# Kernel tuning notes

Measured on AMD Instinct MI355X. Metric: run time of the kernel, lower is better.

The kernel has to match this reference:

```python
import jax, jax.numpy as jnp
import numpy as np
import math

S, B, D, H = 2048, 2, 1024, 16
DK = D // H

def setup_inputs() -> dict:
    key = jax.random.key(0)
    ks = jax.random.split(key, 32)
    f = lambda k, shape, s=1.0: jax.random.normal(k, shape, dtype=jnp.float32) * s
    inp = {
        'qx': f(ks[0], (S, B, D)),
        'kx': f(ks[1], (S, B, D)),
        'vx': f(ks[2], (S, B, D)),
        'qc': f(ks[3], (S, B, D)),
        'kc': f(ks[4], (S, B, D)),
    }
    w = 1.0 / math.sqrt(D)
    names = ['qx_lin', 'kx_lin', 'vx_lin', 'qc_lin', 'kc_lin', 'out_lin']
    for i, n in enumerate(names):
        inp['W_' + n] = f(ks[5 + 2 * i], (D, D), w)
        inp['b_' + n] = f(ks[6 + 2 * i], (D,), w)
    vnames = ['Vqx', 'Vqc', 'Vkx', 'Vkc']
    for i, n in enumerate(vnames):
        inp['W_' + n] = f(ks[17 + 2 * i], (D, 1), w)
        inp['b_' + n] = f(ks[18 + 2 * i], (1,), w)
    return inp

def _forward(qx, kx, vx, qc, kc,
             W_qx_lin, b_qx_lin, W_kx_lin, b_kx_lin, W_vx_lin, b_vx_lin,
             W_qc_lin, b_qc_lin, W_kc_lin, b_kc_lin, W_out_lin, b_out_lin,
             W_Vqx, b_Vqx, W_Vqc, b_Vqc, W_Vkx, b_Vkx, W_Vkc, b_Vkc):
    # [S,B,D] -> [B,S,D]
    qx = jnp.swapaxes(qx, 0, 1)
    kx = jnp.swapaxes(kx, 0, 1)
    vx = jnp.swapaxes(vx, 0, 1)
    qc = jnp.swapaxes(qc, 0, 1)
    kc = jnp.swapaxes(kc, 0, 1)
    bs = qx.shape[0]

    qx = qx @ W_qx_lin + b_qx_lin
    kx = kx @ W_kx_lin + b_kx_lin
    v = vx @ W_vx_lin + b_vx_lin
    qc = qc @ W_qc_lin + b_qc_lin
    kc = kc @ W_kc_lin + b_kc_lin

    lam_q = jax.nn.sigmoid((qx @ W_Vqx + b_Vqx) + (qc @ W_Vqc + b_Vqc))  # [B,S,1]
    lam_k = jax.nn.sigmoid((kx @ W_Vkx + b_Vkx) + (kc @ W_Vkc + b_Vkc))
    q = (1.0 - lam_q) * qx + lam_q * qc
    k = (1.0 - lam_k) * kx + lam_k * kc

    # [B,S,D] -> [B,H,S,dk]
    q = q.reshape(bs, -1, H, DK).transpose(0, 2, 1, 3)
    k = k.reshape(bs, -1, H, DK).transpose(0, 2, 1, 3)
    v = v.reshape(bs, -1, H, DK).transpose(0, 2, 1, 3)

    scores = jnp.einsum('bhqd,bhkd->bhqk', q, k) / math.sqrt(DK)
    attn = jax.nn.softmax(scores, axis=-1)  # dropout is identity in eval
    ctx = jnp.einsum('bhqk,bhkd->bhqd', attn, v)

    concat = ctx.transpose(0, 2, 1, 3).reshape(bs, -1, D)
    out = concat @ W_out_lin + b_out_lin
    return jnp.swapaxes(out, 0, 1)  # back to [S,B,D]

def reference(qx, kx, vx, qc, kc,
              W_qx_lin, b_qx_lin, W_kx_lin, b_kx_lin, W_vx_lin, b_vx_lin,
              W_qc_lin, b_qc_lin, W_kc_lin, b_kc_lin, W_out_lin, b_out_lin,
              W_Vqx, b_Vqx, W_Vqc, b_Vqc, W_Vkx, b_Vkx, W_Vkc, b_Vkc):
    return _forward(qx, kx, vx, qc, kc,
                    W_qx_lin, b_qx_lin, W_kx_lin, b_kx_lin, W_vx_lin, b_vx_lin,
                    W_qc_lin, b_qc_lin, W_kc_lin, b_kc_lin, W_out_lin, b_out_lin,
                    W_Vqx, b_Vqx, W_Vqc, b_Vqc, W_Vkx, b_Vkx, W_Vkc, b_Vkc)
```

## Files before the change

### kernel.cpp

```cpp
#include <hip/hip_runtime.h>
#include <math.h>

typedef unsigned short u16;
typedef __attribute__((ext_vector_type(8))) short short8;
typedef __attribute__((ext_vector_type(4))) float floatx4;
typedef __attribute__((ext_vector_type(4))) unsigned short ushort4v;
typedef __attribute__((ext_vector_type(2))) unsigned int uint2v;

__device__ __forceinline__ float bf2f(u16 x) {
    union { unsigned int u; float f; } v; v.u = ((unsigned int)x) << 16; return v.f;
}
__device__ __forceinline__ u16 f2bf(float f) {
    union { float f; unsigned int u; } v; v.f = f;
    unsigned int r = v.u + 0x7fffu + ((v.u >> 16) & 1u);
    return (u16)(r >> 16);
}
__device__ __forceinline__ unsigned int pk2bf(float a, float b) {
    return (unsigned int)f2bf(a) | ((unsigned int)f2bf(b) << 16);
}

__device__ __forceinline__ void gl_lds16(const void* g, void* l) {
    __builtin_amdgcn_global_load_lds(
        (const __attribute__((address_space(1))) unsigned int*)g,
        (__attribute__((address_space(3))) unsigned int*)l,
        16, 0, 0);
}

struct CastJobs { const float* src[5]; u16* dst[5]; };

__global__ __launch_bounds__(256) void castbf(CastJobs cj) {
    const int z = blockIdx.y;
    const size_t i = (size_t)blockIdx.x * 256 + threadIdx.x;
    const floatx4 v = *(const floatx4*)(cj.src[z] + i * 4);
    ushort4v o;
#pragma unroll
    for (int j = 0; j < 4; j++) o[j] = f2bf(v[j]);
    *(ushort4v*)(cj.dst[z] + i * 4) = o;
}

struct WTJobs { const float* src[6]; u16* dst[6]; };

__global__ __launch_bounds__(256) void wtrans(WTJobs wj) {
    __shared__ float tile[32][33];
    const int z = blockIdx.z;
    const float* W = wj.src[z];
    u16* Wt = wj.dst[z];
    const int n0 = blockIdx.x * 32, k0 = blockIdx.y * 32;
    const int tx = threadIdx.x & 31, ty = threadIdx.x >> 5;
#pragma unroll
    for (int i = 0; i < 4; i++)
        tile[ty + i * 8][tx] = W[(size_t)(k0 + ty + i * 8) * 1024 + n0 + tx];
    __syncthreads();
#pragma unroll
    for (int i = 0; i < 4; i++)
        Wt[(size_t)(n0 + ty + i * 8) * 1024 + k0 + tx] = f2bf(tile[tx][ty + i * 8]);
}

__global__ __launch_bounds__(256) void vtrans(const u16* __restrict__ V,
                                              u16* __restrict__ Vtg) {
    __shared__ u16 tile[32][34];
    const int bh = blockIdx.z, b = bh >> 4, h = bh & 15;
    const int base = b * 1024 + h * 64;
    const int s0 = blockIdx.x * 32, d0 = blockIdx.y * 32;
    const int tx = threadIdx.x & 31, ty = threadIdx.x >> 5;
#pragma unroll
    for (int i = 0; i < 4; i++)
        tile[ty + i * 8][tx] = V[(size_t)(s0 + ty + i * 8) * 2048 + base + d0 + tx];
    __syncthreads();
#pragma unroll
    for (int i = 0; i < 4; i++)
        Vtg[((size_t)bh * 64 + d0 + ty + i * 8) * 2048 + s0 + tx] = tile[tx][ty + i * 8];
}

struct GemmJob { const u16* A; const u16* Bt; const float* bias; u16* Cb; float* Cf; };
struct GemmJobs { GemmJob j[5]; };

__global__ __launch_bounds__(256, 2) void gemm_bt(GemmJobs jobs, int K, int N, int f32out) {
    __shared__ u16 As[128 * 32];
    __shared__ u16 Bs[128 * 32];
    const GemmJob jb = jobs.j[blockIdx.z];
    const int m0 = blockIdx.y * 128;
    const int n0 = blockIdx.x * 128;
    const int t = threadIdx.x;
    const int lane = t & 63;
    const int wid = t >> 6;
    const int wm = wid >> 1, wn = wid & 1;
    const int qd = lane >> 4, lm = lane & 15;

    const floatx4 zero4 = {0.f, 0.f, 0.f, 0.f};
    floatx4 acc[4][4];
#pragma unroll
    for (int i = 0; i < 4; i++)
#pragma unroll
        for (int j2 = 0; j2 < 4; j2++) acc[i][j2] = zero4;

    const u16* Ab = jb.A + (size_t)m0 * K;
    const u16* Bb = jb.Bt + (size_t)n0 * K;
    const int e0 = t * 8;
    const int r0 = e0 >> 5, c0 = e0 & 31;
    const int e1 = (256 + t) * 8;
    const int r1 = e1 >> 5, c1 = e1 & 31;

    for (int k0 = 0; k0 < K; k0 += 32) {
        __syncthreads();
        gl_lds16(Ab + (size_t)r0 * K + k0 + c0, &As[e0]);
        gl_lds16(Ab + (size_t)r1 * K + k0 + c1, &As[e1]);
        gl_lds16(Bb + (size_t)r0 * K + k0 + c0, &Bs[e0]);
        gl_lds16(Bb + (size_t)r1 * K + k0 + c1, &Bs[e1]);
        __syncthreads();

        short8 af[4], bfg[4];
#pragma unroll
        for (int i = 0; i < 4; i++) {
            af[i]  = *(const short8*)&As[(wm * 64 + i * 16 + lm) * 32 + qd * 8];
            bfg[i] = *(const short8*)&Bs[(wn * 64 + i * 16 + lm) * 32 + qd * 8];
        }
#pragma unroll
        for (int i = 0; i < 4; i++)
#pragma unroll
            for (int j2 = 0; j2 < 4; j2++)
                acc[i][j2] = __builtin_amdgcn_mfma_f32_16x16x32_bf16(af[i], bfg[j2], acc[i][j2], 0, 0, 0);
    }

#pragma unroll
    for (int i = 0; i < 4; i++) {
        const int mb = m0 + wm * 64 + i * 16 + qd * 4;
#pragma unroll
        for (int j2 = 0; j2 < 4; j2++) {
            const int col = n0 + wn * 64 + j2 * 16 + lm;
            const float bv = jb.bias[col];
            const floatx4 c = acc[i][j2];
            if (f32out) {
#pragma unroll
                for (int r = 0; r < 4; r++)
                    jb.Cf[(size_t)(mb + r) * N + col] = c[r] + bv;
            } else {
#pragma unroll
                for (int r = 0; r < 4; r++)
                    jb.Cb[(size_t)(mb + r) * N + col] = f2bf(c[r] + bv);
            }
        }
    }
}

__global__ __launch_bounds__(256) void gating(
    const u16* __restrict__ qxp, const u16* __restrict__ qcp,
    const u16* __restrict__ kxp, const u16* __restrict__ kcp,
    const float* __restrict__ wVqx, const float* __restrict__ wVqc,
    const float* __restrict__ wVkx, const float* __restrict__ wVkc,
    const float* __restrict__ bVqx, const float* __restrict__ bVqc,
    const float* __restrict__ bVkx, const float* __restrict__ bVkc,
    u16* __restrict__ qg, u16* __restrict__ kg) {
    const int row = blockIdx.x;
    const int z = blockIdx.y;
    const u16* xa = z ? kxp : qxp;
    const u16* xb = z ? kcp : qcp;
    const float* wa = z ? wVkx : wVqx;
    const float* wb = z ? wVkc : wVqc;
    const float bsum = z ? (bVkx[0] + bVkc[0]) : (bVqx[0] + bVqc[0]);
    u16* out = z ? kg : qg;

    const int t = threadIdx.x;
    const size_t off = (size_t)row * 1024 + t * 4;
    const ushort4v av = *(const ushort4v*)(xa + off);
    const ushort4v bv = *(const ushort4v*)(xb + off);
    const floatx4 wav = *(const floatx4*)(wa + t * 4);
    const floatx4 wbv = *(const floatx4*)(wb + t * 4);
    float afl[4], bfl[4];
    float part = 0.f;
#pragma unroll
    for (int j = 0; j < 4; j++) {
        afl[j] = bf2f(av[j]); bfl[j] = bf2f(bv[j]);
        part += afl[j] * wav[j] + bfl[j] * wbv[j];
    }
#pragma unroll
    for (int m = 1; m <= 32; m <<= 1) part += __shfl_xor(part, m);
    __shared__ float red[4];
    if ((t & 63) == 0) red[t >> 6] = part;
    __syncthreads();
    const float tot = red[0] + red[1] + red[2] + red[3] + bsum;
    const float lam = 1.f / (1.f + exp2f(-tot * 1.44269504f));
    ushort4v ov;
#pragma unroll
    for (int j = 0; j < 4; j++) ov[j] = f2bf(afl[j] + lam * (bfl[j] - afl[j]));
    *(ushort4v*)(out + off) = ov;
}

__global__ __launch_bounds__(256, 2) void attn2(
    const u16* __restrict__ Q, const u16* __restrict__ Kk,
    const u16* __restrict__ Vtg, u16* __restrict__ O) {
    __shared__ u16 Ks[64 * 72];
    __shared__ u16 Vs[64 * 72];
    __shared__ u16 Ps[4 * 32 * 72];

    const int bh = blockIdx.y, b = bh >> 4, h = bh & 15;
    const int base = b * 1024 + h * 64;
    const int t = threadIdx.x, lane = t & 63, w = t >> 6;
    const int qd = lane >> 4, lm = lane & 15;
    const int q0 = blockIdx.x * 128 + w * 32;

    short8 qf[2][2];
#pragma unroll
    for (int qh = 0; qh < 2; qh++) {
        const u16* qr = Q + (size_t)(q0 + qh * 16 + lm) * 2048 + base;
#pragma unroll
        for (int c = 0; c < 2; c++)
            qf[qh][c] = *(const short8*)(qr + c * 32 + qd * 8);
    }

    const floatx4 zero4 = {0.f, 0.f, 0.f, 0.f};
    floatx4 ctx[2][4];
#pragma unroll
    for (int qh = 0; qh < 2; qh++)
#pragma unroll
        for (int g = 0; g < 4; g++) ctx[qh][g] = zero4;
    float lpart[2] = {0.f, 0.f};

    u16* Pw = &Ps[w * 32 * 72];
    const float C = 0.18033688011112042f;

    const int sr = t >> 3, sc = (t & 7) * 8;
    const u16* ksrc = Kk + (size_t)sr * 2048 + base + sc;
    const u16* vsrc = Vtg + ((size_t)bh * 64 + sr) * 2048 + sc;
    u16* kdst0 = &Ks[sr * 72 + sc];
    u16* kdst1 = &Ks[(sr + 32) * 72 + sc];
    u16* vdst0 = &Vs[sr * 72 + sc];
    u16* vdst1 = &Vs[(sr + 32) * 72 + sc];

    for (int kt = 0; kt < 32; kt++) {
        __syncthreads();
        *(short8*)kdst0 = *(const short8*)ksrc;
        *(short8*)kdst1 = *(const short8*)(ksrc + (size_t)32 * 2048);
        *(short8*)vdst0 = *(const short8*)vsrc;
        *(short8*)vdst1 = *(const short8*)(vsrc + (size_t)32 * 2048);
        ksrc += (size_t)64 * 2048;
        vsrc += 64;
        __syncthreads();

#pragma unroll
        for (int g = 0; g < 4; g++) {
            const short8 kf0 = *(const short8*)&Ks[(g * 16 + lm) * 72 + qd * 8];
            const short8 kf1 = *(const short8*)&Ks[(g * 16 + lm) * 72 + 32 + qd * 8];
#pragma unroll
            for (int qh = 0; qh < 2; qh++) {
                floatx4 st = zero4;
                st = __builtin_amdgcn_mfma_f32_16x16x32_bf16(kf0, qf[qh][0], st, 0, 0, 0);
                st = __builtin_amdgcn_mfma_f32_16x16x32_bf16(kf1, qf[qh][1], st, 0, 0, 0);
                float p0 = exp2f(st[0] * C);
                float p1 = exp2f(st[1] * C);
                float p2 = exp2f(st[2] * C);
                float p3 = exp2f(st[3] * C);
                lpart[qh] += (p0 + p1) + (p2 + p3);
                uint2v pw;
                pw[0] = pk2bf(p0, p1);
                pw[1] = pk2bf(p2, p3);
                *(uint2v*)&Pw[(qh * 16 + lm) * 72 + g * 16 + qd * 4] = pw;
            }
        }

        short8 pa[2][2];
#pragma unroll
        for (int qh = 0; qh < 2; qh++)
#pragma unroll
            for (int c = 0; c < 2; c++)
                pa[qh][c] = *(const short8*)&Pw[(qh * 16 + lm) * 72 + c * 32 + qd * 8];
#pragma unroll
        for (int g = 0; g < 4; g++) {
            const short8 vb0 = *(const short8*)&Vs[(g * 16 + lm) * 72 + qd * 8];
            const short8 vb1 = *(const short8*)&Vs[(g * 16 + lm) * 72 + 32 + qd * 8];
#pragma unroll
            for (int qh = 0; qh < 2; qh++) {
                ctx[qh][g] = __builtin_amdgcn_mfma_f32_16x16x32_bf16(pa[qh][0], vb0, ctx[qh][g], 0, 0, 0);
                ctx[qh][g] = __builtin_amdgcn_mfma_f32_16x16x32_bf16(pa[qh][1], vb1, ctx[qh][g], 0, 0, 0);
            }
        }
    }

#pragma unroll
    for (int qh = 0; qh < 2; qh++) {
        float l = lpart[qh];
        l += __shfl_xor(l, 16);
        l += __shfl_xor(l, 32);
        float linv[4];
#pragma unroll
        for (int r = 0; r < 4; r++)
            linv[r] = 1.0f / __shfl(l, qd * 4 + r);
#pragma unroll
        for (int r = 0; r < 4; r++) {
            const int srow = q0 + qh * 16 + qd * 4 + r;
            u16* orow = O + (size_t)srow * 2048 + base;
#pragma unroll
            for (int g = 0; g < 4; g++)
                orow[g * 16 + lm] = f2bf(ctx[qh][g][r] * linv[r]);
        }
    }
}

extern "C" void kernel_launch(void* const* d_in, const int* in_sizes, int n_in,
                              void* d_out, int out_size, void* d_ws, size_t ws_size,
                              hipStream_t stream) {
    const float* qx = (const float*)d_in[0];
    const float* kx = (const float*)d_in[1];
    const float* vx = (const float*)d_in[2];
    const float* qc = (const float*)d_in[3];
    const float* kc = (const float*)d_in[4];
    const float* W_qx = (const float*)d_in[5];   const float* b_qx = (const float*)d_in[6];
    const float* W_kx = (const float*)d_in[7];   const float* b_kx = (const float*)d_in[8];
    const float* W_vx = (const float*)d_in[9];   const float* b_vx = (const float*)d_in[10];
    const float* W_qc = (const float*)d_in[11];  const float* b_qc = (const float*)d_in[12];
    const float* W_kc = (const float*)d_in[13];  const float* b_kc = (const float*)d_in[14];
    const float* W_out = (const float*)d_in[15]; const float* b_out = (const float*)d_in[16];
    const float* W_Vqx = (const float*)d_in[17]; const float* b_Vqx = (const float*)d_in[18];
    const float* W_Vqc = (const float*)d_in[19]; const float* b_Vqc = (const float*)d_in[20];
    const float* W_Vkx = (const float*)d_in[21]; const float* b_Vkx = (const float*)d_in[22];
    const float* W_Vkc = (const float*)d_in[23]; const float* b_Vkc = (const float*)d_in[24];

    char* ws = (char*)d_ws;
    const size_t NT = 4194304;
    const size_t XB_OFF = 0;
    const size_t WT_OFF = XB_OFF + 5 * NT * 2;
    const size_t P_OFF  = WT_OFF + 6 * 2097152;
    const size_t QG_OFF = P_OFF + 5 * NT * 2;
    const size_t KG_OFF = QG_OFF + NT * 2;
    const size_t CTX_OFF = KG_OFF + NT * 2;

    u16* Xb[5];
    for (int i = 0; i < 5; i++) Xb[i] = (u16*)(ws + XB_OFF + (size_t)i * NT * 2);
    u16* Wt[6];
    for (int i = 0; i < 6; i++) Wt[i] = (u16*)(ws + WT_OFF + (size_t)i * 2097152);
    u16* P[5];
    for (int i = 0; i < 5; i++) P[i] = (u16*)(ws + P_OFF + (size_t)i * NT * 2);
    u16* qg  = (u16*)(ws + QG_OFF);
    u16* kg  = (u16*)(ws + KG_OFF);
    u16* ctx = (u16*)(ws + CTX_OFF);
    u16* Vtg = (u16*)(ws + XB_OFF);

    CastJobs cj;
    const float* srcs[5] = {qx, kx, vx, qc, kc};
    for (int i = 0; i < 5; i++) { cj.src[i] = srcs[i]; cj.dst[i] = Xb[i]; }
    castbf<<<dim3(4096, 5), 256, 0, stream>>>(cj);

    WTJobs wj;
    const float* wsrc[6] = {W_qx, W_kx, W_vx, W_qc, W_kc, W_out};
    for (int i = 0; i < 6; i++) { wj.src[i] = wsrc[i]; wj.dst[i] = Wt[i]; }
    wtrans<<<dim3(32, 32, 6), 256, 0, stream>>>(wj);

    GemmJobs gj;
    const float* biases[5] = {b_qx, b_kx, b_vx, b_qc, b_kc};
    for (int i = 0; i < 5; i++) {
        gj.j[i].A = Xb[i]; gj.j[i].Bt = Wt[i]; gj.j[i].bias = biases[i];
        gj.j[i].Cb = P[i]; gj.j[i].Cf = nullptr;
    }
    gemm_bt<<<dim3(8, 32, 5), 256, 0, stream>>>(gj, 1024, 1024, 0);

    gating<<<dim3(4096, 2), 256, 0, stream>>>(P[0], P[3], P[1], P[4],
        W_Vqx, W_Vqc, W_Vkx, W_Vkc, b_Vqx, b_Vqc, b_Vkx, b_Vkc, qg, kg);

    vtrans<<<dim3(64, 2, 32), 256, 0, stream>>>(P[2], Vtg);

    attn2<<<dim3(16, 32), 256, 0, stream>>>(qg, kg, Vtg, ctx);

    GemmJobs gf;
    for (int i = 0; i < 5; i++) {
        gf.j[i].A = ctx; gf.j[i].Bt = Wt[5]; gf.j[i].bias = b_out;
        gf.j[i].Cb = nullptr; gf.j[i].Cf = (float*)d_out;
    }
    gemm_bt<<<dim3(8, 32, 1), 256, 0, stream>>>(gf, 1024, 1024, 1);
}
```

Baseline: 390.2 us.

## Fuse gating into dual projection GEMM and split attention over KV halves

Computes the gating lambdas algebraically: W·v is precomputed and dotted with the raw fp32 inputs in the cast kernel, so lambda is known before the projections. A new dual-GEMM kernel computes the x and c projections together and blends them in its epilogue. This removes the separate gating pass and the bf16 intermediates for q and k. Attention is split into two KV halves to double the grid, with a merge kernel that adds the fp32 partials, at the cost of extra fp32 traffic and two added launches. Lambda is now taken from fp32 inputs rather than bf16 projections, which slightly changes the numerics.

```diff
diff --git a/kernel.cpp b/kernel.cpp
--- a/kernel.cpp
+++ b/kernel.cpp
@@ -16,7 +16,12 @@
     return (u16)(r >> 16);
 }
 __device__ __forceinline__ unsigned int pk2bf(float a, float b) {
+#if __has_builtin(__builtin_amdgcn_cvt_pk_bf16_f32)
+    auto r = __builtin_amdgcn_cvt_pk_bf16_f32(a, b);
+    union { decltype(r) v; unsigned int u; } cv; cv.v = r; return cv.u;
+#else
     return (unsigned int)f2bf(a) | ((unsigned int)f2bf(b) << 16);
+#endif
 }
 
 __device__ __forceinline__ void gl_lds16(const void* g, void* l) {
@@ -26,16 +31,86 @@
         16, 0, 0);
 }
 
-struct CastJobs { const float* src[5]; u16* dst[5]; };
+struct WFuseJobs { const float* W[4]; const float* wv[4]; float* out[4]; };
+
+__global__ __launch_bounds__(256) void wfuse(WFuseJobs wf) {
+    const int z = blockIdx.y;
+    const float* W = wf.W[z];
+    const float* wv = wf.wv[z];
+    float* out = wf.out[z];
+    const int lane = threadIdx.x & 63, w = threadIdx.x >> 6;
+#pragma unroll
+    for (int i = 0; i < 4; i++) {
+        const int row = blockIdx.x * 16 + w * 4 + i;
+        const float* Wr = W + (size_t)row * 1024 + lane * 16;
+        const float* vr = wv + lane * 16;
+        float p = 0.f;
+#pragma unroll
+        for (int c = 0; c < 4; c++) {
+            const floatx4 a = *(const floatx4*)(Wr + c * 4);
+            const floatx4 b = *(const floatx4*)(vr + c * 4);
+            p += a[0] * b[0] + a[1] * b[1] + a[2] * b[2] + a[3] * b[3];
+        }
+#pragma unroll
+        for (int m = 1; m <= 32; m <<= 1) p += __shfl_xor(p, m);
+        if (lane == 0) out[row] = p;
+    }
+}
+
+struct CastJobs { const float* src[5]; u16* dst[5]; const float* w[5]; float* dot[5]; };
 
 __global__ __launch_bounds__(256) void castbf(CastJobs cj) {
     const int z = blockIdx.y;
-    const size_t i = (size_t)blockIdx.x * 256 + threadIdx.x;
+    const int row = blockIdx.x;
+    const int t = threadIdx.x;
+    const size_t i = (size_t)row * 256 + t;
     const floatx4 v = *(const floatx4*)(cj.src[z] + i * 4);
     ushort4v o;
 #pragma unroll
     for (int j = 0; j < 4; j++) o[j] = f2bf(v[j]);
     *(ushort4v*)(cj.dst[z] + i * 4) = o;
+
+    if (cj.w[z]) {
+        const floatx4 wv = *(const floatx4*)(cj.w[z] + t * 4);
+        float p = v[0] * wv[0] + v[1] * wv[1] + v[2] * wv[2] + v[3] * wv[3];
+#pragma unroll
+        for (int m = 1; m <= 32; m <<= 1) p += __shfl_xor(p, m);
+        __shared__ float red[4];
+        if ((t & 63) == 0) red[t >> 6] = p;
+        __syncthreads();
+        if (t == 0) cj.dot[z][row] = red[0] + red[1] + red[2] + red[3];
+    }
+}
+
+struct LamJobs {
+    const float* dA[2]; const float* dB[2];
+    const float* b1[2]; const float* b2[2];
+    const float* wv1[2]; const float* wv2[2];
+    const float* s1[2]; const float* s2[2];
+    float* lam[2];
+};
+
+__global__ __launch_bounds__(256) void lamk(LamJobs lj) {
+    const int z = blockIdx.y;
+    const int t = threadIdx.x;
+    float p = 0.f;
+    {
+        const floatx4 a1 = *(const floatx4*)(lj.b1[z] + t * 4);
+        const floatx4 w1 = *(const floatx4*)(lj.wv1[z] + t * 4);
+        const floatx4 a2 = *(const floatx4*)(lj.b2[z] + t * 4);
+        const floatx4 w2 = *(const floatx4*)(lj.wv2[z] + t * 4);
+#pragma unroll
+        for (int j = 0; j < 4; j++) p += a1[j] * w1[j] + a2[j] * w2[j];
+    }
+#pragma unroll
+    for (int m = 1; m <= 32; m <<= 1) p += __shfl_xor(p, m);
+    __shared__ float red[4];
+    if ((t & 63) == 0) red[t >> 6] = p;
+    __syncthreads();
+    const float c = red[0] + red[1] + red[2] + red[3] + lj.s1[z][0] + lj.s2[z][0];
+    const int row = blockIdx.x * 256 + t;
+    const float x = lj.dA[z][row] + lj.dB[z][row] + c;
+    lj.lam[z][row] = 1.f / (1.f + exp2f(-x * 1.44269504f));
 }
 
 struct WTJobs { const float* src[6]; u16* dst[6]; };
@@ -73,7 +148,7 @@
 }
 
 struct GemmJob { const u16* A; const u16* Bt; const float* bias; u16* Cb; float* Cf; };
-struct GemmJobs { GemmJob j[5]; };
+struct GemmJobs { GemmJob j[1]; };
 
 __global__ __launch_bounds__(256, 2) void gemm_bt(GemmJobs jobs, int K, int N, int f32out) {
     __shared__ u16 As[128 * 32];
@@ -143,57 +218,103 @@
     }
 }
 
-__global__ __launch_bounds__(256) void gating(
-    const u16* __restrict__ qxp, const u16* __restrict__ qcp,
-    const u16* __restrict__ kxp, const u16* __restrict__ kcp,
-    const float* __restrict__ wVqx, const float* __restrict__ wVqc,
-    const float* __restrict__ wVkx, const float* __restrict__ wVkc,
-    const float* __restrict__ bVqx, const float* __restrict__ bVqc,
-    const float* __restrict__ bVkx, const float* __restrict__ bVkc,
-    u16* __restrict__ qg, u16* __restrict__ kg) {
-    const int row = blockIdx.x;
-    const int z = blockIdx.y;
-    const u16* xa = z ? kxp : qxp;
-    const u16* xb = z ? kcp : qcp;
-    const float* wa = z ? wVkx : wVqx;
-    const float* wb = z ? wVkc : wVqc;
-    const float bsum = z ? (bVkx[0] + bVkc[0]) : (bVqx[0] + bVqc[0]);
-    u16* out = z ? kg : qg;
-
+struct FuseJob {
+    const u16* Aa; const u16* Ac; const u16* Ba; const u16* Bc;
+    const float* biasA; const float* biasC; const float* lam; u16* out;
+};
+struct FuseJobs { FuseJob j[2]; };
+
+__global__ __launch_bounds__(256, 2) void fusedproj(FuseJobs jobs) {
+    __shared__ u16 Asa[128 * 32];
+    __shared__ u16 Asc[128 * 32];
+    __shared__ u16 Bsa[128 * 32];
+    __shared__ u16 Bsc[128 * 32];
+    const FuseJob jb = jobs.j[blockIdx.z];
+    const int K = 1024;
+    const int m0 = blockIdx.y * 128;
+    const int n0 = blockIdx.x * 128;
     const int t = threadIdx.x;
-    const size_t off = (size_t)row * 1024 + t * 4;
-    const ushort4v av = *(const ushort4v*)(xa + off);
-    const ushort4v bv = *(const ushort4v*)(xb + off);
-    const floatx4 wav = *(const floatx4*)(wa + t * 4);
-    const floatx4 wbv = *(const floatx4*)(wb + t * 4);
-    float afl[4], bfl[4];
-    float part = 0.f;
-#pragma unroll
-    for (int j = 0; j < 4; j++) {
-        afl[j] = bf2f(av[j]); bfl[j] = bf2f(bv[j]);
-        part += afl[j] * wav[j] + bfl[j] * wbv[j];
-    }
-#pragma unroll
-    for (int m = 1; m <= 32; m <<= 1) part += __shfl_xor(part, m);
-    __shared__ float red[4];
-    if ((t & 63) == 0) red[t >> 6] = part;
-    __syncthreads();
-    const float tot = red[0] + red[1] + red[2] + red[3] + bsum;
-    const float lam = 1.f / (1.f + exp2f(-tot * 1.44269504f));
-    ushort4v ov;
-#pragma unroll
-    for (int j = 0; j < 4; j++) ov[j] = f2bf(afl[j] + lam * (bfl[j] - afl[j]));
-    *(ushort4v*)(out + off) = ov;
-}
-
-__global__ __launch_bounds__(256, 2) void attn2(
+    const int lane = t & 63;
+    const int wid = t >> 6;
+    const int wm = wid >> 1, wn = wid & 1;
+    const int qd = lane >> 4, lm = lane & 15;
+
+    const floatx4 zero4 = {0.f, 0.f, 0.f, 0.f};
+    floatx4 accA[4][4], accC[4][4];
+#pragma unroll
+    for (int i = 0; i < 4; i++)
+#pragma unroll
+        for (int j2 = 0; j2 < 4; j2++) { accA[i][j2] = zero4; accC[i][j2] = zero4; }
+
+    const u16* Aab = jb.Aa + (size_t)m0 * K;
+    const u16* Acb = jb.Ac + (size_t)m0 * K;
+    const u16* Bab = jb.Ba + (size_t)n0 * K;
+    const u16* Bcb = jb.Bc + (size_t)n0 * K;
+    const int e0 = t * 8;
+    const int r0 = e0 >> 5, c0 = e0 & 31;
+    const int e1 = (256 + t) * 8;
+    const int r1 = e1 >> 5, c1 = e1 & 31;
+
+    for (int k0 = 0; k0 < K; k0 += 32) {
+        __syncthreads();
+        gl_lds16(Aab + (size_t)r0 * K + k0 + c0, &Asa[e0]);
+        gl_lds16(Aab + (size_t)r1 * K + k0 + c1, &Asa[e1]);
+        gl_lds16(Acb + (size_t)r0 * K + k0 + c0, &Asc[e0]);
+        gl_lds16(Acb + (size_t)r1 * K + k0 + c1, &Asc[e1]);
+        gl_lds16(Bab + (size_t)r0 * K + k0 + c0, &Bsa[e0]);
+        gl_lds16(Bab + (size_t)r1 * K + k0 + c1, &Bsa[e1]);
+        gl_lds16(Bcb + (size_t)r0 * K + k0 + c0, &Bsc[e0]);
+        gl_lds16(Bcb + (size_t)r1 * K + k0 + c1, &Bsc[e1]);
+        __syncthreads();
+
+        short8 aa[4], ac[4], ba[4], bc[4];
+#pragma unroll
+        for (int i = 0; i < 4; i++) {
+            aa[i] = *(const short8*)&Asa[(wm * 64 + i * 16 + lm) * 32 + qd * 8];
+            ac[i] = *(const short8*)&Asc[(wm * 64 + i * 16 + lm) * 32 + qd * 8];
+            ba[i] = *(const short8*)&Bsa[(wn * 64 + i * 16 + lm) * 32 + qd * 8];
+            bc[i] = *(const short8*)&Bsc[(wn * 64 + i * 16 + lm) * 32 + qd * 8];
+        }
+#pragma unroll
+        for (int i = 0; i < 4; i++)
+#pragma unroll
+            for (int j2 = 0; j2 < 4; j2++) {
+                accA[i][j2] = __builtin_amdgcn_mfma_f32_16x16x32_bf16(aa[i], ba[j2], accA[i][j2], 0, 0, 0);
+                accC[i][j2] = __builtin_amdgcn_mfma_f32_16x16x32_bf16(ac[i], bc[j2], accC[i][j2], 0, 0, 0);
+            }
+    }
+
+#pragma unroll
+    for (int i = 0; i < 4; i++) {
+        const int mb = m0 + wm * 64 + i * 16 + qd * 4;
+        float lamv[4];
+#pragma unroll
+        for (int r = 0; r < 4; r++) lamv[r] = jb.lam[mb + r];
+#pragma unroll
+        for (int j2 = 0; j2 < 4; j2++) {
+            const int col = n0 + wn * 64 + j2 * 16 + lm;
+            const float bA = jb.biasA[col];
+            const float bC = jb.biasC[col];
+#pragma unroll
+            for (int r = 0; r < 4; r++) {
+                const float va = accA[i][j2][r] + bA;
+                const float vc = accC[i][j2][r] + bC;
+                jb.out[(size_t)(mb + r) * 1024 + col] = f2bf(va + lamv[r] * (vc - va));
+            }
+        }
+    }
+}
+
+__global__ __launch_bounds__(256, 2) void attn3(
     const u16* __restrict__ Q, const u16* __restrict__ Kk,
-    const u16* __restrict__ Vtg, u16* __restrict__ O) {
+    const u16* __restrict__ Vtg, float* __restrict__ ctxp,
+    float* __restrict__ lp) {
     __shared__ u16 Ks[64 * 72];
     __shared__ u16 Vs[64 * 72];
     __shared__ u16 Ps[4 * 32 * 72];
 
     const int bh = blockIdx.y, b = bh >> 4, h = bh & 15;
+    const int sp = blockIdx.z;
     const int base = b * 1024 + h * 64;
     const int t = threadIdx.x, lane = t & 63, w = t >> 6;
     const int qd = lane >> 4, lm = lane & 15;
@@ -220,14 +341,14 @@
     const float C = 0.18033688011112042f;
 
     const int sr = t >> 3, sc = (t & 7) * 8;
-    const u16* ksrc = Kk + (size_t)sr * 2048 + base + sc;
-    const u16* vsrc = Vtg + ((size_t)bh * 64 + sr) * 2048 + sc;
+    const u16* ksrc = Kk + (size_t)(sp * 1024 + sr) * 2048 + base + sc;
+    const u16* vsrc = Vtg + ((size_t)bh * 64 + sr) * 2048 + sp * 1024 + sc;
     u16* kdst0 = &Ks[sr * 72 + sc];
     u16* kdst1 = &Ks[(sr + 32) * 72 + sc];
     u16* vdst0 = &Vs[sr * 72 + sc];
     u16* vdst1 = &Vs[(sr + 32) * 72 + sc];
 
-    for (int kt = 0; kt < 32; kt++) {
+    for (int kt = 0; kt < 16; kt++) {
         __syncthreads();
         *(short8*)kdst0 = *(const short8*)ksrc;
         *(short8*)kdst1 = *(const short8*)(ksrc + (size_t)32 * 2048);
@@ -246,10 +367,10 @@
                 floatx4 st = zero4;
                 st = __builtin_amdgcn_mfma_f32_16x16x32_bf16(kf0, qf[qh][0], st, 0, 0, 0);
                 st = __builtin_amdgcn_mfma_f32_16x16x32_bf16(kf1, qf[qh][1], st, 0, 0, 0);
-                float p0 = exp2f(st[0] * C);
-                float p1 = exp2f(st[1] * C);
-                float p2 = exp2f(st[2] * C);
-                float p3 = exp2f(st[3] * C);
+                const float p0 = exp2f(st[0] * C);
+                const float p1 = exp2f(st[1] * C);
+                const float p2 = exp2f(st[2] * C);
+                const float p3 = exp2f(st[3] * C);
                 lpart[qh] += (p0 + p1) + (p2 + p3);
                 uint2v pw;
                 pw[0] = pk2bf(p0, p1);
@@ -276,24 +397,42 @@
         }
     }
 
+    float* cbase = ctxp + (size_t)sp * 4194304;
 #pragma unroll
     for (int qh = 0; qh < 2; qh++) {
         float l = lpart[qh];
         l += __shfl_xor(l, 16);
         l += __shfl_xor(l, 32);
-        float linv[4];
-#pragma unroll
-        for (int r = 0; r < 4; r++)
-            linv[r] = 1.0f / __shfl(l, qd * 4 + r);
+        if (lane < 16)
+            lp[(size_t)sp * 65536 + bh * 2048 + q0 + qh * 16 + lane] = l;
 #pragma unroll
         for (int r = 0; r < 4; r++) {
             const int srow = q0 + qh * 16 + qd * 4 + r;
-            u16* orow = O + (size_t)srow * 2048 + base;
+            float* orow = cbase + (size_t)srow * 2048 + base;
 #pragma unroll
             for (int g = 0; g < 4; g++)
-                orow[g * 16 + lm] = f2bf(ctx[qh][g][r] * linv[r]);
-        }
-    }
+                orow[g * 16 + lm] = ctx[qh][g][r];
+        }
+    }
+}
+
+__global__ __launch_bounds__(256) void merge(const float* __restrict__ ctxp,
+                                             const float* __restrict__ lp,
+                                             u16* __restrict__ out) {
+    const size_t idx = ((size_t)blockIdx.x * 256 + threadIdx.x) * 4;
+    const floatx4 a = *(const floatx4*)(ctxp + idx);
+    const floatx4 c = *(const floatx4*)(ctxp + 4194304 + idx);
+    const int srow = (int)(idx >> 11);
+    const int rem = (int)(idx & 2047);
+    const int bh = rem >> 6;
+    const float l = lp[bh * 2048 + srow] + lp[65536 + bh * 2048 + srow];
+    const float inv = 1.0f / l;
+    ushort4v o;
+    const unsigned int lo = pk2bf((a[0] + c[0]) * inv, (a[1] + c[1]) * inv);
+    const unsigned int hi = pk2bf((a[2] + c[2]) * inv, (a[3] + c[3]) * inv);
+    o[0] = (u16)(lo & 0xffff); o[1] = (u16)(lo >> 16);
+    o[2] = (u16)(hi & 0xffff); o[3] = (u16)(hi >> 16);
+    *(ushort4v*)(out + idx) = o;
 }
 
 extern "C" void kernel_launch(void* const* d_in, const int* in_sizes, int n_in,
@@ -317,53 +456,72 @@
 
     char* ws = (char*)d_ws;
     const size_t NT = 4194304;
-    const size_t XB_OFF = 0;
-    const size_t WT_OFF = XB_OFF + 5 * NT * 2;
-    const size_t P_OFF  = WT_OFF + 6 * 2097152;
-    const size_t QG_OFF = P_OFF + 5 * NT * 2;
-    const size_t KG_OFF = QG_OFF + NT * 2;
-    const size_t CTX_OFF = KG_OFF + NT * 2;
-
+    const size_t MB = 1048576;
     u16* Xb[5];
-    for (int i = 0; i < 5; i++) Xb[i] = (u16*)(ws + XB_OFF + (size_t)i * NT * 2);
+    for (int i = 0; i < 5; i++) Xb[i] = (u16*)(ws + (size_t)i * NT * 2);
     u16* Wt[6];
-    for (int i = 0; i < 6; i++) Wt[i] = (u16*)(ws + WT_OFF + (size_t)i * 2097152);
-    u16* P[5];
-    for (int i = 0; i < 5; i++) P[i] = (u16*)(ws + P_OFF + (size_t)i * NT * 2);
-    u16* qg  = (u16*)(ws + QG_OFF);
-    u16* kg  = (u16*)(ws + KG_OFF);
-    u16* ctx = (u16*)(ws + CTX_OFF);
-    u16* Vtg = (u16*)(ws + XB_OFF);
+    for (int i = 0; i < 6; i++) Wt[i] = (u16*)(ws + 40 * MB + (size_t)i * 2 * MB);
+    u16* Pv    = (u16*)(ws + 52 * MB);
+    u16* qg    = (u16*)(ws + 60 * MB);
+    u16* kg    = (u16*)(ws + 68 * MB);
+    u16* ctxbf = (u16*)(ws + 76 * MB);
+    float* wfused = (float*)(ws + 84 * MB);
+    float* dots   = (float*)(ws + 84 * MB + 16384);
+    float* lam    = (float*)(ws + 84 * MB + 16384 + 65536);
+    float* l_part = (float*)(ws + 84 * MB + 16384 + 65536 + 32768);
+    float* ctxp = (float*)ws;
+    u16* Vtg    = (u16*)(ws + 32 * MB);
+
+    WFuseJobs wf;
+    wf.W[0] = W_qx; wf.wv[0] = W_Vqx; wf.out[0] = wfused;
+    wf.W[1] = W_qc; wf.wv[1] = W_Vqc; wf.out[1] = wfused + 1024;
+    wf.W[2] = W_kx; wf.wv[2] = W_Vkx; wf.out[2] = wfused + 2048;
+    wf.W[3] = W_kc; wf.wv[3] = W_Vkc; wf.out[3] = wfused + 3072;
+    wfuse<<<dim3(64, 4), 256, 0, stream>>>(wf);
 
     CastJobs cj;
     const float* srcs[5] = {qx, kx, vx, qc, kc};
-    for (int i = 0; i < 5; i++) { cj.src[i] = srcs[i]; cj.dst[i] = Xb[i]; }
+    for (int i = 0; i < 5; i++) { cj.src[i] = srcs[i]; cj.dst[i] = Xb[i]; cj.w[i] = nullptr; cj.dot[i] = nullptr; }
+    cj.w[0] = wfused;        cj.dot[0] = dots;
+    cj.w[3] = wfused + 1024; cj.dot[3] = dots + 4096;
+    cj.w[1] = wfused + 2048; cj.dot[1] = dots + 8192;
+    cj.w[4] = wfused + 3072; cj.dot[4] = dots + 12288;
     castbf<<<dim3(4096, 5), 256, 0, stream>>>(cj);
+
+    LamJobs lj;
+    lj.dA[0] = dots;        lj.dB[0] = dots + 4096;
+    lj.b1[0] = b_qx; lj.b2[0] = b_qc; lj.wv1[0] = W_Vqx; lj.wv2[0] = W_Vqc;
+    lj.s1[0] = b_Vqx; lj.s2[0] = b_Vqc; lj.lam[0] = lam;
+    lj.dA[1] = dots + 8192; lj.dB[1] = dots + 12288;
+    lj.b1[1] = b_kx; lj.b2[1] = b_kc; lj.wv1[1] = W_Vkx; lj.wv2[1] = W_Vkc;
+    lj.s1[1] = b_Vkx; lj.s2[1] = b_Vkc; lj.lam[1] = lam + 4096;
+    lamk<<<dim3(16, 2), 256, 0, stream>>>(lj);
 
     WTJobs wj;
     const float* wsrc[6] = {W_qx, W_kx, W_vx, W_qc, W_kc, W_out};
     for (int i = 0; i < 6; i++) { wj.src[i] = wsrc[i]; wj.dst[i] = Wt[i]; }
     wtrans<<<dim3(32, 32, 6), 256, 0, stream>>>(wj);
 
-    GemmJobs gj;
-    const float* biases[5] = {b_qx, b_kx, b_vx, b_qc, b_kc};
-    for (int i = 0; i < 5; i++) {
-        gj.j[i].A = Xb[i]; gj.j[i].Bt = Wt[i]; gj.j[i].bias = biases[i];
-        gj.j[i].Cb = P[i]; gj.j[i].Cf = nullptr;
-    }
-    gemm_bt<<<dim3(8, 32, 5), 256, 0, stream>>>(gj, 1024, 1024, 0);
-
-    gating<<<dim3(4096, 2), 256, 0, stream>>>(P[0], P[3], P[1], P[4],
-        W_Vqx, W_Vqc, W_Vkx, W_Vkc, b_Vqx, b_Vqc, b_Vkx, b_Vkc, qg, kg);
-
-    vtrans<<<dim3(64, 2, 32), 256, 0, stream>>>(P[2], Vtg);
-
-    attn2<<<dim3(16, 32), 256, 0, stream>>>(qg, kg, Vtg, ctx);
+    FuseJobs fj;
+    fj.j[0].Aa = Xb[0]; fj.j[0].Ac = Xb[3]; fj.j[0].Ba = Wt[0]; fj.j[0].Bc = Wt[3];
+    fj.j[0].biasA = b_qx; fj.j[0].biasC = b_qc; fj.j[0].lam = lam;        fj.j[0].out = qg;
+    fj.j[1].Aa = Xb[1]; fj.j[1].Ac = Xb[4]; fj.j[1].Ba = Wt[1]; fj.j[1].Bc = Wt[4];
+    fj.j[1].biasA = b_kx; fj.j[1].biasC = b_kc; fj.j[1].lam = lam + 4096; fj.j[1].out = kg;
+    fusedproj<<<dim3(8, 32, 2), 256, 0, stream>>>(fj);
+
+    GemmJobs gv;
+    gv.j[0].A = Xb[2]; gv.j[0].Bt = Wt[2]; gv.j[0].bias = b_vx;
+    gv.j[0].Cb = Pv; gv.j[0].Cf = nullptr;
+    gemm_bt<<<dim3(8, 32, 1), 256, 0, stream>>>(gv, 1024, 1024, 0);
+
+    vtrans<<<dim3(64, 2, 32), 256, 0, stream>>>(Pv, Vtg);
+
+    attn3<<<dim3(16, 32, 2), 256, 0, stream>>>(qg, kg, Vtg, ctxp, l_part);
+
+    merge<<<4096, 256, 0, stream>>>(ctxp, l_part, ctxbf);
 
     GemmJobs gf;
-    for (int i = 0; i < 5; i++) {
-        gf.j[i].A = ctx; gf.j[i].Bt = Wt[5]; gf.j[i].bias = b_out;
-        gf.j[i].Cb = nullptr; gf.j[i].Cf = (float*)d_out;
-    }
+    gf.j[0].A = ctxbf; gf.j[0].Bt = Wt[5]; gf.j[0].bias = b_out;
+    gf.j[0].Cb = nullptr; gf.j[0].Cf = (float*)d_out;
     gemm_bt<<<dim3(8, 32, 1), 256, 0, stream>>>(gf, 1024, 1024, 1);
 }
```

After: 388.9 us. Within noise of the previous version (-0.3%).
